# Optimization experiments

Measured on AMD Instinct MI355X. Metric: run time of the kernel, lower is better.

Reference implementation:

```python
import jax, jax.numpy as jnp
import numpy as np

TOP_K = 2
NUM_EXPERTS = 8
LB_COEFF = 0.01


def setup_inputs() -> dict:
    key = jax.random.key(0)
    ks = jax.random.split(key, 5)
    B, S, D, F, E = 4, 2048, 1024, 4096, NUM_EXPERTS
    s_in = 0.02
    return {
        "x": jax.random.normal(ks[0], (B, S, D), jnp.float32),
        "gate_w": jax.random.normal(ks[1], (D, E), jnp.float32) * s_in,
        "gate_b": jnp.zeros((E,), jnp.float32),
        "fc1_w": jax.random.normal(ks[2], (E, D, 2 * F), jnp.float32) * s_in,
        "fc1_b": jnp.zeros((E, 2 * F), jnp.float32),
        "fc2_w": jax.random.normal(ks[3], (E, F, D), jnp.float32) * s_in,
        "fc2_b": jnp.zeros((E, D), jnp.float32),
    }


def reference(x, gate_w, gate_b, fc1_w, fc1_b, fc2_w, fc2_b):
    B, S, D = x.shape
    E = gate_w.shape[1]
    xt = x.reshape(-1, D)                      # [T, D]
    T = xt.shape[0]

    gate_logits = xt @ gate_w + gate_b        # [T, E]
    gate_probs = jax.nn.softmax(gate_logits, axis=-1)
    top_w, top_i = jax.lax.top_k(gate_probs, TOP_K)      # [T, K]
    w_norm = top_w / (top_w.sum(-1, keepdims=True) + 1e-6)

    rows = jnp.arange(T)[:, None]
    # per-token per-expert combine weight (0 if expert not in top-k)
    combine = jnp.zeros((T, E), xt.dtype).at[rows, top_i].add(w_norm)  # [T, E]

    out = jnp.zeros_like(xt)
    for e in range(E):  # fixed small expert loop; each is a dense GEMM
        h = xt @ fc1_w[e] + fc1_b[e]                      # [T, 2F]
        a, g = jnp.split(h, 2, axis=-1)
        act = a * jax.nn.gelu(g, approximate=False)       # SwiGLU (exact gelu, torch default)
        y = act @ fc2_w[e] + fc2_b[e]                     # [T, D]
        out = out + combine[:, e:e + 1] * y

    chosen_mask = jnp.zeros((T, E), gate_probs.dtype).at[rows, top_i].set(1.0)
    frac = chosen_mask.mean(0)
    mean_probs = gate_probs.mean(0)
    lb_loss = LB_COEFF * E * jnp.sum(frac * mean_probs)

    return out.reshape(B, S, D), lb_loss
```

## Files before the change

### kernel.cpp

```cpp
#include <hip/hip_runtime.h>
#include <hip/hip_bf16.h>
#include <stdint.h>

typedef __attribute__((ext_vector_type(4))) float f32x4;
typedef __attribute__((ext_vector_type(8))) __bf16 bf16x8;
typedef __attribute__((ext_vector_type(4))) unsigned short u16x4;
typedef unsigned short u16;

#define NTOK 8192
#define DDIM 1024
#define FDIM 4096
#define NEXP 8

#define WS_XB    0ull
#define WS_W1T   (16777216ull)
#define WS_W2T   (WS_W1T + 134217728ull)
#define WS_ACT   (WS_W2T + 67108864ull)
#define WS_LIST  (WS_ACT + 142606336ull)
#define WS_PAIRW (WS_LIST + 262144ull)
#define WS_CNT   (WS_PAIRW + 262144ull)
#define WS_SUMP  (WS_CNT + 32ull)
#define WS_PAD   (WS_SUMP + 32ull)
#define WS_OFF   (WS_PAD + 32ull)
#define WS_T1E   (WS_OFF + 32ull)
#define WS_T1R   (WS_T1E + 512ull)
#define WS_T2E   (WS_T1R + 512ull)
#define WS_T2R   (WS_T2E + 1024ull)

static __device__ __forceinline__ u16 bf16rne(float f) {
  union { float f; uint32_t u; } c; c.f = f;
  return (u16)((c.u + 0x7FFFu + ((c.u >> 16) & 1u)) >> 16);
}

static __device__ __forceinline__ void load_lds16(const void* g, void* l) {
  __builtin_amdgcn_global_load_lds((const __attribute__((address_space(1))) void*)g,
                                   (__attribute__((address_space(3))) void*)l, 16, 0, 0);
}

__global__ __launch_bounds__(256) void gate_kernel(
    const float* __restrict__ x, const float* __restrict__ gw,
    const float* __restrict__ gb, u16* __restrict__ xb,
    int* __restrict__ cnt, float* __restrict__ sump,
    int* __restrict__ list, float* __restrict__ pairw) {
  const int tid = threadIdx.x;
  const int lane = tid & 63;
  const int wv = tid >> 6;
  const int t = blockIdx.x * 4 + wv;

  __shared__ float sp[8];
  if (tid < 8) sp[tid] = 0.f;
  __syncthreads();

  float acc[8] = {0.f,0.f,0.f,0.f,0.f,0.f,0.f,0.f};
  const float4* x4 = (const float4*)x + (size_t)t * 256;
  u16x4* xb4 = (u16x4*)xb + (size_t)t * 256;
  #pragma unroll
  for (int it = 0; it < 4; ++it) {
    const float4 xv = x4[it * 64 + lane];
    u16x4 bv;
    bv[0] = bf16rne(xv.x); bv[1] = bf16rne(xv.y);
    bv[2] = bf16rne(xv.z); bv[3] = bf16rne(xv.w);
    xb4[it * 64 + lane] = bv;
    const int d0 = (it * 64 + lane) * 4;
    #pragma unroll
    for (int j = 0; j < 4; ++j) {
      const float xs = (j == 0) ? xv.x : ((j == 1) ? xv.y : ((j == 2) ? xv.z : xv.w));
      const float* g = gw + (size_t)(d0 + j) * 8;
      #pragma unroll
      for (int e2 = 0; e2 < 8; ++e2) acc[e2] += xs * g[e2];
    }
  }
  #pragma unroll
  for (int e2 = 0; e2 < 8; ++e2) {
    float v = acc[e2];
    v += __shfl_xor(v, 1);  v += __shfl_xor(v, 2);  v += __shfl_xor(v, 4);
    v += __shfl_xor(v, 8);  v += __shfl_xor(v, 16); v += __shfl_xor(v, 32);
    acc[e2] = v;
  }
  float p[8]; float mx = -1e30f;
  #pragma unroll
  for (int e2 = 0; e2 < 8; ++e2) { p[e2] = acc[e2] + gb[e2]; mx = fmaxf(mx, p[e2]); }
  float s = 0.f;
  #pragma unroll
  for (int e2 = 0; e2 < 8; ++e2) { p[e2] = expf(p[e2] - mx); s += p[e2]; }
  const float inv = 1.f / s;
  #pragma unroll
  for (int e2 = 0; e2 < 8; ++e2) p[e2] *= inv;

  if (lane == 0) {
    int i1 = 0; float v1 = p[0];
    #pragma unroll
    for (int e2 = 1; e2 < 8; ++e2) if (p[e2] > v1) { v1 = p[e2]; i1 = e2; }
    int i2 = 0; float v2 = -1.f;
    #pragma unroll
    for (int e2 = 0; e2 < 8; ++e2) if (e2 != i1 && p[e2] > v2) { v2 = p[e2]; i2 = e2; }
    const float den = v1 + v2 + 1e-6f;
    const int p1 = atomicAdd(&cnt[i1], 1);
    list[i1 * NTOK + p1] = t; pairw[i1 * NTOK + p1] = v1 / den;
    const int p2 = atomicAdd(&cnt[i2], 1);
    list[i2 * NTOK + p2] = t; pairw[i2 * NTOK + p2] = v2 / den;
    #pragma unroll
    for (int e2 = 0; e2 < 8; ++e2) atomicAdd(&sp[e2], p[e2]);
  }
  __syncthreads();
  if (tid < 8) atomicAdd(&sump[tid], sp[tid]);
}

__global__ __launch_bounds__(256) void conv_transpose(
    const float* __restrict__ in, u16* __restrict__ out, int R, int C) {
  __shared__ float tile[64][65];
  const int e = blockIdx.z;
  const float* pin = in + (size_t)e * R * C;
  u16* pout = out + (size_t)e * R * C;
  const int tx = threadIdx.x & 15;
  const int ty = threadIdx.x >> 4;
  const int c0 = blockIdx.x * 64;
  const int r0 = blockIdx.y * 64;
  #pragma unroll
  for (int i = 0; i < 4; ++i) {
    const int r = ty + i * 16;
    const float4 v = *(const float4*)(pin + (size_t)(r0 + r) * C + c0 + tx * 4);
    tile[r][tx * 4 + 0] = v.x;
    tile[r][tx * 4 + 1] = v.y;
    tile[r][tx * 4 + 2] = v.z;
    tile[r][tx * 4 + 3] = v.w;
  }
  __syncthreads();
  #pragma unroll
  for (int i = 0; i < 4; ++i) {
    const int c = ty + i * 16;
    u16x4 o;
    o[0] = bf16rne(tile[tx * 4 + 0][c]);
    o[1] = bf16rne(tile[tx * 4 + 1][c]);
    o[2] = bf16rne(tile[tx * 4 + 2][c]);
    o[3] = bf16rne(tile[tx * 4 + 3][c]);
    *(u16x4*)(pout + (size_t)(c0 + c) * R + r0 + tx * 4) = o;
  }
}

__global__ void route_finalize(const int* __restrict__ cnt, const float* __restrict__ sump,
                               int* __restrict__ padc, int* __restrict__ offs,
                               int* __restrict__ list, float* __restrict__ pairw,
                               int* __restrict__ t1e, int* __restrict__ t1r,
                               int* __restrict__ t2e, int* __restrict__ t2r,
                               float* __restrict__ lb_out) {
  __shared__ int s_c[8], s_p[8];
  const int tid = threadIdx.x;
  if (tid == 0) {
    int o = 0; float lb = 0.f;
    for (int e = 0; e < 8; ++e) {
      const int c = cnt[e];
      const int pc = (c + 127) & ~127;
      s_c[e] = c; s_p[e] = pc;
      padc[e] = pc; offs[e] = o; o += pc;
      lb += ((float)c / 8192.f) * (sump[e] / 8192.f);
    }
    lb_out[0] = 0.01f * 8.f * lb;
    int n1 = 0;
    for (int e = 0; e < 8; ++e)
      for (int r = 0; r < s_p[e]; r += 256) { t1e[n1] = e; t1r[n1] = r; ++n1; }
    for (; n1 < 72; ++n1) { t1e[n1] = -1; t1r[n1] = 0; }
    int n2 = 0;
    for (int e = 0; e < 8; ++e)
      for (int r = 0; r < s_p[e]; r += 256) { t2e[n2] = e; t2r[n2] = r; ++n2; }
    for (; n2 < 72; ++n2) { t2e[n2] = -1; t2r[n2] = 0; }
  }
  __syncthreads();
  for (int e = 0; e < 8; ++e)
    for (int pq = s_c[e] + tid; pq < s_p[e]; pq += blockDim.x) {
      list[e * NTOK + pq] = 0; pairw[e * NTOK + pq] = 0.f;
    }
}

#define G1_NT 16
__global__ __launch_bounds__(512, 2) void gemm1_kernel(
    const u16* __restrict__ xb, const u16* __restrict__ w1t,
    const float* __restrict__ b1, const int* __restrict__ list,
    const int* __restrict__ padc, const int* __restrict__ offs,
    const int* __restrict__ t1e, const int* __restrict__ t1r,
    u16* __restrict__ act) {
  const int tt = blockIdx.y;
  const int e = t1e[tt];
  if (e < 0) return;
  const int row0 = t1r[tt];
  const int j = blockIdx.x;
  const int pc = padc[e];
  const int off_e = offs[e];

  __shared__ u16 lds[65536];

  const int tid = threadIdx.x;
  const int lane = tid & 63;
  const int wv = tid >> 6;
  const int wr = wv >> 2, wc = wv & 3;
  const int l15 = lane & 15, l4 = lane >> 4;

  const int rt0 = tid >> 2, rt1 = rt0 + 128;
  const int ce = ((tid & 3) ^ ((rt0 >> 1) & 3)) * 8;
  const int slot0 = row0 + rt0, slot1 = row0 + rt1;
  const int tok0 = (slot0 < pc) ? list[e * NTOK + slot0] : 0;
  const int tok1 = (slot1 < pc) ? list[e * NTOK + slot1] : 0;
  const u16* srcA0 = xb + (size_t)tok0 * DDIM + ce;
  const u16* srcA1 = xb + (size_t)tok1 * DDIM + ce;
  const int gn0 = j * 128 + (rt0 >> 5) * 16 + (rt0 & 15) + ((rt0 >> 4) & 1) * FDIM;
  const int gn1 = j * 128 + (rt1 >> 5) * 16 + (rt1 & 15) + ((rt1 >> 4) & 1) * FDIM;
  const u16* srcB0 = w1t + ((size_t)e * 2 * FDIM + gn0) * DDIM + ce;
  const u16* srcB1 = w1t + ((size_t)e * 2 * FDIM + gn1) * DDIM + ce;

  const int kel = (l4 ^ ((l15 >> 1) & 3)) * 8;
  const int aBase = (wr * 128 + l15) * 32 + kel;
  const int bBase = (wc * 64 + l15) * 32 + kel;

  f32x4 acc[8][4];
  #pragma unroll
  for (int m = 0; m < 8; ++m)
    #pragma unroll
    for (int n = 0; n < 4; ++n) { acc[m][n][0]=0.f; acc[m][n][1]=0.f; acc[m][n][2]=0.f; acc[m][n][3]=0.f; }

  #define STAGE_A(buf, kk, kt) do { \
    u16* _d = &lds[(buf) * 16384 + (kk) * 8192 + wv * 512]; \
    load_lds16(srcA0 + (kt) * 64 + (kk) * 32, _d); \
    load_lds16(srcA1 + (kt) * 64 + (kk) * 32, _d + 4096); \
  } while (0)
  #define STAGE_B(buf, kk, kt) do { \
    u16* _d = &lds[32768 + (buf) * 16384 + (kk) * 8192 + wv * 512]; \
    load_lds16(srcB0 + (kt) * 64 + (kk) * 32, _d); \
    load_lds16(srcB1 + (kt) * 64 + (kk) * 32, _d + 4096); \
  } while (0)

  STAGE_A(0, 0, 0); STAGE_B(0, 0, 0); STAGE_A(0, 1, 0); STAGE_B(0, 1, 0);
  STAGE_A(1, 0, 1); STAGE_B(1, 0, 1); STAGE_A(1, 1, 1);
  asm volatile("s_waitcnt vmcnt(6)" ::: "memory");
  __builtin_amdgcn_s_barrier();

  bf16x8 aF[8];
  for (int t = 0; t < G1_NT; ++t) {
    const int cur = t & 1;
    const int Ac0 = cur * 16384, Ac1 = Ac0 + 8192;
    const int Bc0 = 32768 + cur * 16384, Bc1 = Bc0 + 8192;
    {
      #pragma unroll
      for (int m = 0; m < 8; ++m) aF[m] = *(const bf16x8*)&lds[Ac0 + aBase + m * 512];
      bf16x8 b0 = *(const bf16x8*)&lds[Bc0 + bBase + 0 * 512];
      bf16x8 b1f = *(const bf16x8*)&lds[Bc0 + bBase + 1 * 512];
      __builtin_amdgcn_sched_barrier(0);
      if (t + 1 < G1_NT) STAGE_B(cur ^ 1, 1, t + 1);
      __builtin_amdgcn_s_barrier();
      __builtin_amdgcn_s_setprio(1);
      #pragma unroll
      for (int m = 0; m < 8; ++m) {
        acc[m][0] = __builtin_amdgcn_mfma_f32_16x16x32_bf16(aF[m], b0, acc[m][0], 0, 0, 0);
        acc[m][1] = __builtin_amdgcn_mfma_f32_16x16x32_bf16(aF[m], b1f, acc[m][1], 0, 0, 0);
      }
      __builtin_amdgcn_s_setprio(0);
      __builtin_amdgcn_s_barrier();
    }
    {
      bf16x8 b2 = *(const bf16x8*)&lds[Bc0 + bBase + 2 * 512];
      bf16x8 b3 = *(const bf16x8*)&lds[Bc0 + bBase + 3 * 512];
      __builtin_amdgcn_sched_barrier(0);
      if (t + 2 < G1_NT) STAGE_A(cur, 0, t + 2);
      __builtin_amdgcn_s_barrier();
      __builtin_amdgcn_s_setprio(1);
      #pragma unroll
      for (int m = 0; m < 8; ++m) {
        acc[m][2] = __builtin_amdgcn_mfma_f32_16x16x32_bf16(aF[m], b2, acc[m][2], 0, 0, 0);
        acc[m][3] = __builtin_amdgcn_mfma_f32_16x16x32_bf16(aF[m], b3, acc[m][3], 0, 0, 0);
      }
      __builtin_amdgcn_s_setprio(0);
      __builtin_amdgcn_s_barrier();
    }
    {
      #pragma unroll
      for (int m = 0; m < 8; ++m) aF[m] = *(const bf16x8*)&lds[Ac1 + aBase + m * 512];
      bf16x8 b0 = *(const bf16x8*)&lds[Bc1 + bBase + 0 * 512];
      bf16x8 b1f = *(const bf16x8*)&lds[Bc1 + bBase + 1 * 512];
      __builtin_amdgcn_sched_barrier(0);
      if (t + 2 < G1_NT) STAGE_B(cur, 0, t + 2);
      __builtin_amdgcn_s_barrier();
      __builtin_amdgcn_s_setprio(1);
      #pragma unroll
      for (int m = 0; m < 8; ++m) {
        acc[m][0] = __builtin_amdgcn_mfma_f32_16x16x32_bf16(aF[m], b0, acc[m][0], 0, 0, 0);
        acc[m][1] = __builtin_amdgcn_mfma_f32_16x16x32_bf16(aF[m], b1f, acc[m][1], 0, 0, 0);
      }
      __builtin_amdgcn_s_setprio(0);
      __builtin_amdgcn_s_barrier();
    }
    {
      bf16x8 b2 = *(const bf16x8*)&lds[Bc1 + bBase + 2 * 512];
      bf16x8 b3 = *(const bf16x8*)&lds[Bc1 + bBase + 3 * 512];
      __builtin_amdgcn_sched_barrier(0);
      if (t + 2 < G1_NT) STAGE_A(cur, 1, t + 2);
      __builtin_amdgcn_s_barrier();
      __builtin_amdgcn_s_setprio(1);
      #pragma unroll
      for (int m = 0; m < 8; ++m) {
        acc[m][2] = __builtin_amdgcn_mfma_f32_16x16x32_bf16(aF[m], b2, acc[m][2], 0, 0, 0);
        acc[m][3] = __builtin_amdgcn_mfma_f32_16x16x32_bf16(aF[m], b3, acc[m][3], 0, 0, 0);
      }
      __builtin_amdgcn_s_setprio(0);
      if (t < G1_NT - 1) {
        if (t == G1_NT - 2) asm volatile("s_waitcnt vmcnt(0)" ::: "memory");
        else                asm volatile("s_waitcnt vmcnt(6)" ::: "memory");
      }
      __builtin_amdgcn_s_barrier();
    }
  }
  #undef STAGE_A
  #undef STAGE_B

  const int rowlim = pc - row0;
  const size_t actrow0 = (size_t)(off_e + row0);
  #pragma unroll
  for (int p2 = 0; p2 < 2; ++p2) {
    const int col = j * 128 + (wc * 2 + p2) * 16 + l15;
    const float ba = b1[e * (2 * FDIM) + col];
    const float bg = b1[e * (2 * FDIM) + FDIM + col];
    #pragma unroll
    for (int m = 0; m < 8; ++m) {
      #pragma unroll
      for (int jr = 0; jr < 4; ++jr) {
        const int row = wr * 128 + m * 16 + l4 * 4 + jr;
        if (row < rowlim) {
          const float a = acc[m][2 * p2][jr] + ba;
          const float g = acc[m][2 * p2 + 1][jr] + bg;
          const float u = 0.7978845608028654f * (g + 0.044715f * g * g * g);
          const float ex = __expf(2.f * u);
          const float th = 1.f - 2.f / (ex + 1.f);
          const float gg = 0.5f * g * (1.f + th);
          act[(actrow0 + row) * FDIM + col] = bf16rne(a * gg);
        }
      }
    }
  }
}

#define G2_NT 64
__global__ __launch_bounds__(512, 2) void gemm2_kernel(
    const u16* __restrict__ act, const u16* __restrict__ w2t,
    const float* __restrict__ b2, const int* __restrict__ list,
    const float* __restrict__ pairw, const int* __restrict__ padc,
    const int* __restrict__ offs,
    const int* __restrict__ t2e, const int* __restrict__ t2r,
    float* __restrict__ out) {
  const int tt = blockIdx.x;
  const int e = t2e[tt];
  if (e < 0) return;
  const int row0 = t2r[tt];
  const int jt = blockIdx.y;
  const int pc = padc[e];
  const int off_e = offs[e];

  __shared__ u16 lds[49152];

  const int tid = threadIdx.x;
  const int lane = tid & 63;
  const int wv = tid >> 6;
  const int wr = wv >> 2, wc = wv & 3;
  const int l15 = lane & 15, l4 = lane >> 4;

  const int rt0 = tid >> 2, rt1 = rt0 + 128;
  const int ce = ((tid & 3) ^ ((rt0 >> 1) & 3)) * 8;
  const u16* srcA0 = act + (size_t)(off_e + row0 + rt0) * FDIM + ce;
  const u16* srcA1 = act + (size_t)(off_e + row0 + rt1) * FDIM + ce;
  const u16* srcB0 = w2t + ((size_t)e * DDIM + jt * 128 + rt0) * FDIM + ce;

  const int kel = (l4 ^ ((l15 >> 1) & 3)) * 8;
  const int aBase = (wr * 128 + l15) * 32 + kel;
  const int bBase = (wc * 32 + l15) * 32 + kel;

  f32x4 acc[8][2];
  #pragma unroll
  for (int m = 0; m < 8; ++m)
    #pragma unroll
    for (int n = 0; n < 2; ++n) { acc[m][n][0]=0.f; acc[m][n][1]=0.f; acc[m][n][2]=0.f; acc[m][n][3]=0.f; }

  #define STAGE2_A(buf, kk, kt) do { \
    u16* _d = &lds[(buf) * 16384 + (kk) * 8192 + wv * 512]; \
    load_lds16(srcA0 + (kt) * 64 + (kk) * 32, _d); \
    load_lds16(srcA1 + (kt) * 64 + (kk) * 32, _d + 4096); \
  } while (0)
  #define STAGE2_B(buf, kk, kt) do { \
    u16* _d = &lds[32768 + (buf) * 8192 + (kk) * 4096 + wv * 512]; \
    load_lds16(srcB0 + (kt) * 64 + (kk) * 32, _d); \
  } while (0)

  STAGE2_B(0, 0, 0); STAGE2_A(0, 0, 0); STAGE2_B(0, 1, 0); STAGE2_A(0, 1, 0);
  STAGE2_B(1, 0, 1); STAGE2_A(1, 0, 1); STAGE2_B(1, 1, 1);
  asm volatile("s_waitcnt vmcnt(4)" ::: "memory");
  __builtin_amdgcn_s_barrier();

  bf16x8 aF0[4], aF1[4];
  for (int t = 0; t < G2_NT; ++t) {
    const int cur = t & 1;
    const int Ac0 = cur * 16384, Ac1 = Ac0 + 8192;
    const int Bc0 = 32768 + cur * 8192, Bc1 = Bc0 + 4096;
    bf16x8 b0, b1f;
    {
      #pragma unroll
      for (int m = 0; m < 4; ++m) aF0[m] = *(const bf16x8*)&lds[Ac0 + aBase + m * 512];
      b0  = *(const bf16x8*)&lds[Bc0 + bBase + 0 * 512];
      b1f = *(const bf16x8*)&lds[Bc0 + bBase + 1 * 512];
      __builtin_amdgcn_sched_barrier(0);
      if (t + 1 < G2_NT) STAGE2_A(cur ^ 1, 1, t + 1);
      __builtin_amdgcn_s_barrier();
      __builtin_amdgcn_s_setprio(1);
      #pragma unroll
      for (int m = 0; m < 4; ++m) {
        acc[m][0] = __builtin_amdgcn_mfma_f32_16x16x32_bf16(aF0[m], b0, acc[m][0], 0, 0, 0);
        acc[m][1] = __builtin_amdgcn_mfma_f32_16x16x32_bf16(aF0[m], b1f, acc[m][1], 0, 0, 0);
      }
      __builtin_amdgcn_s_setprio(0);
      __builtin_amdgcn_s_barrier();
    }
    {
      #pragma unroll
      for (int m = 0; m < 4; ++m) aF1[m] = *(const bf16x8*)&lds[Ac0 + aBase + (m + 4) * 512];
      __builtin_amdgcn_sched_barrier(0);
      if (t + 2 < G2_NT) STAGE2_B(cur, 0, t + 2);
      __builtin_amdgcn_s_barrier();
      __builtin_amdgcn_s_setprio(1);
      #pragma unroll
      for (int m = 0; m < 4; ++m) {
        acc[m + 4][0] = __builtin_amdgcn_mfma_f32_16x16x32_bf16(aF1[m], b0, acc[m + 4][0], 0, 0, 0);
        acc[m + 4][1] = __builtin_amdgcn_mfma_f32_16x16x32_bf16(aF1[m], b1f, acc[m + 4][1], 0, 0, 0);
      }
      __builtin_amdgcn_s_setprio(0);
      __builtin_amdgcn_s_barrier();
    }
    {
      #pragma unroll
      for (int m = 0; m < 4; ++m) aF0[m] = *(const bf16x8*)&lds[Ac1 + aBase + m * 512];
      b0  = *(const bf16x8*)&lds[Bc1 + bBase + 0 * 512];
      b1f = *(const bf16x8*)&lds[Bc1 + bBase + 1 * 512];
      __builtin_amdgcn_sched_barrier(0);
      if (t + 2 < G2_NT) STAGE2_A(cur, 0, t + 2);
      __builtin_amdgcn_s_barrier();
      __builtin_amdgcn_s_setprio(1);
      #pragma unroll
      for (int m = 0; m < 4; ++m) {
        acc[m][0] = __builtin_amdgcn_mfma_f32_16x16x32_bf16(aF0[m], b0, acc[m][0], 0, 0, 0);
        acc[m][1] = __builtin_amdgcn_mfma_f32_16x16x32_bf16(aF0[m], b1f, acc[m][1], 0, 0, 0);
      }
      __builtin_amdgcn_s_setprio(0);
      __builtin_amdgcn_s_barrier();
    }
    {
      #pragma unroll
      for (int m = 0; m < 4; ++m) aF1[m] = *(const bf16x8*)&lds[Ac1 + aBase + (m + 4) * 512];
      __builtin_amdgcn_sched_barrier(0);
      if (t + 2 < G2_NT) STAGE2_B(cur, 1, t + 2);
      __builtin_amdgcn_s_barrier();
      __builtin_amdgcn_s_setprio(1);
      #pragma unroll
      for (int m = 0; m < 4; ++m) {
        acc[m + 4][0] = __builtin_amdgcn_mfma_f32_16x16x32_bf16(aF1[m], b0, acc[m + 4][0], 0, 0, 0);
        acc[m + 4][1] = __builtin_amdgcn_mfma_f32_16x16x32_bf16(aF1[m], b1f, acc[m + 4][1], 0, 0, 0);
      }
      __builtin_amdgcn_s_setprio(0);
      if (t < G2_NT - 1) {
        if (t == G2_NT - 2) asm volatile("s_waitcnt vmcnt(0)" ::: "memory");
        else                asm volatile("s_waitcnt vmcnt(4)" ::: "memory");
      }
      __builtin_amdgcn_s_barrier();
    }
  }
  #undef STAGE2_A
  #undef STAGE2_B

  const int rowlim = pc - row0;
  #pragma unroll
  for (int m = 0; m < 8; ++m) {
    #pragma unroll
    for (int jr = 0; jr < 4; ++jr) {
      const int row = wr * 128 + m * 16 + l4 * 4 + jr;
      if (row < rowlim) {
        const int pos = row0 + row;
        const int tok = list[e * NTOK + pos];
        const float pw = pairw[e * NTOK + pos];
        if (pw != 0.f) {
          #pragma unroll
          for (int n = 0; n < 2; ++n) {
            const int col = jt * 128 + wc * 32 + n * 16 + l15;
            const float v = (acc[m][n][jr] + b2[e * DDIM + col]) * pw;
            atomicAdd(&out[(size_t)tok * DDIM + col], v);
          }
        }
      }
    }
  }
}

extern "C" void kernel_launch(void* const* d_in, const int* in_sizes, int n_in,
                              void* d_out, int out_size, void* d_ws, size_t ws_size,
                              hipStream_t stream) {
  const float* x   = (const float*)d_in[0];
  const float* gw  = (const float*)d_in[1];
  const float* gb  = (const float*)d_in[2];
  const float* f1w = (const float*)d_in[3];
  const float* f1b = (const float*)d_in[4];
  const float* f2w = (const float*)d_in[5];
  const float* f2b = (const float*)d_in[6];
  float* out = (float*)d_out;
  char* ws = (char*)d_ws;

  u16*   xb    = (u16*)(ws + WS_XB);
  u16*   w1t   = (u16*)(ws + WS_W1T);
  u16*   w2t   = (u16*)(ws + WS_W2T);
  u16*   act   = (u16*)(ws + WS_ACT);
  int*   list  = (int*)(ws + WS_LIST);
  float* pairw = (float*)(ws + WS_PAIRW);
  int*   cnt   = (int*)(ws + WS_CNT);
  float* sump  = (float*)(ws + WS_SUMP);
  int*   padc  = (int*)(ws + WS_PAD);
  int*   offs  = (int*)(ws + WS_OFF);
  int*   t1e   = (int*)(ws + WS_T1E);
  int*   t1r   = (int*)(ws + WS_T1R);
  int*   t2e   = (int*)(ws + WS_T2E);
  int*   t2r   = (int*)(ws + WS_T2R);

  (void)hipMemsetAsync(d_out, 0, (size_t)out_size * sizeof(float), stream);
  (void)hipMemsetAsync(ws + WS_CNT, 0, 64, stream);

  gate_kernel<<<NTOK / 4, 256, 0, stream>>>(x, gw, gb, xb, cnt, sump, list, pairw);
  conv_transpose<<<dim3(8192 / 64, 1024 / 64, 8), 256, 0, stream>>>(f1w, w1t, 1024, 8192);
  conv_transpose<<<dim3(1024 / 64, 4096 / 64, 8), 256, 0, stream>>>(f2w, w2t, 4096, 1024);
  route_finalize<<<1, 256, 0, stream>>>(cnt, sump, padc, offs, list, pairw,
                                        t1e, t1r, t2e, t2r, out + 8388608);
  gemm1_kernel<<<dim3(32, 72), 512, 0, stream>>>(xb, w1t, f1b, list, padc, offs, t1e, t1r, act);
  gemm2_kernel<<<dim3(72, 8), 512, 0, stream>>>(act, w2t, f2b, list, pairw, padc, offs, t2e, t2r, out);
}
```

Baseline: 1.090 ms.

## Software-pipeline LDS fragment loads across phases in both GEMMs and swap gemm2 grid axes

Both GEMM main loops are restructured so each phase computes on fragments loaded in an earlier phase. The next tile's A (and, in gemm2, B) fragments are prefetched from LDS after the final barrier so their latency overlaps MFMA work. Gemm1 now uses a 4x4 register-blocked pattern over M halves instead of 8x2 over N halves. Gemm2's grid is transposed so blocks sharing an activation row tile launch adjacently, which should improve L2 reuse of the act rows. The prefetching raises register pressure and depends on the barrier ordering staying correct.

Result: no change. 1.092 ms (+0.2%).

```diff
diff --git a/kernel.cpp b/kernel.cpp
--- a/kernel.cpp
+++ b/kernel.cpp
@@ -233,77 +233,85 @@
   asm volatile("s_waitcnt vmcnt(6)" ::: "memory");
   __builtin_amdgcn_s_barrier();
 
-  bf16x8 aF[8];
+  bf16x8 aLo[4], aHi[4];
+  bf16x8 bk[4];
+  #pragma unroll
+  for (int m = 0; m < 4; ++m) aLo[m] = *(const bf16x8*)&lds[0 + aBase + m * 512];
+  __builtin_amdgcn_sched_barrier(0);
+
   for (int t = 0; t < G1_NT; ++t) {
     const int cur = t & 1;
     const int Ac0 = cur * 16384, Ac1 = Ac0 + 8192;
     const int Bc0 = 32768 + cur * 16384, Bc1 = Bc0 + 8192;
     {
       #pragma unroll
-      for (int m = 0; m < 8; ++m) aF[m] = *(const bf16x8*)&lds[Ac0 + aBase + m * 512];
-      bf16x8 b0 = *(const bf16x8*)&lds[Bc0 + bBase + 0 * 512];
-      bf16x8 b1f = *(const bf16x8*)&lds[Bc0 + bBase + 1 * 512];
+      for (int n = 0; n < 4; ++n) bk[n] = *(const bf16x8*)&lds[Bc0 + bBase + n * 512];
+      #pragma unroll
+      for (int m = 0; m < 4; ++m) aHi[m] = *(const bf16x8*)&lds[Ac0 + aBase + (m + 4) * 512];
       __builtin_amdgcn_sched_barrier(0);
       if (t + 1 < G1_NT) STAGE_B(cur ^ 1, 1, t + 1);
       __builtin_amdgcn_s_barrier();
       __builtin_amdgcn_s_setprio(1);
       #pragma unroll
-      for (int m = 0; m < 8; ++m) {
-        acc[m][0] = __builtin_amdgcn_mfma_f32_16x16x32_bf16(aF[m], b0, acc[m][0], 0, 0, 0);
-        acc[m][1] = __builtin_amdgcn_mfma_f32_16x16x32_bf16(aF[m], b1f, acc[m][1], 0, 0, 0);
-      }
-      __builtin_amdgcn_s_setprio(0);
-      __builtin_amdgcn_s_barrier();
-    }
-    {
-      bf16x8 b2 = *(const bf16x8*)&lds[Bc0 + bBase + 2 * 512];
-      bf16x8 b3 = *(const bf16x8*)&lds[Bc0 + bBase + 3 * 512];
+      for (int m = 0; m < 4; ++m)
+        #pragma unroll
+        for (int n = 0; n < 4; ++n)
+          acc[m][n] = __builtin_amdgcn_mfma_f32_16x16x32_bf16(aLo[m], bk[n], acc[m][n], 0, 0, 0);
+      __builtin_amdgcn_s_setprio(0);
+      __builtin_amdgcn_s_barrier();
+    }
+    {
+      #pragma unroll
+      for (int m = 0; m < 4; ++m) aLo[m] = *(const bf16x8*)&lds[Ac1 + aBase + m * 512];
       __builtin_amdgcn_sched_barrier(0);
       if (t + 2 < G1_NT) STAGE_A(cur, 0, t + 2);
       __builtin_amdgcn_s_barrier();
       __builtin_amdgcn_s_setprio(1);
       #pragma unroll
-      for (int m = 0; m < 8; ++m) {
-        acc[m][2] = __builtin_amdgcn_mfma_f32_16x16x32_bf16(aF[m], b2, acc[m][2], 0, 0, 0);
-        acc[m][3] = __builtin_amdgcn_mfma_f32_16x16x32_bf16(aF[m], b3, acc[m][3], 0, 0, 0);
-      }
-      __builtin_amdgcn_s_setprio(0);
-      __builtin_amdgcn_s_barrier();
-    }
-    {
-      #pragma unroll
-      for (int m = 0; m < 8; ++m) aF[m] = *(const bf16x8*)&lds[Ac1 + aBase + m * 512];
-      bf16x8 b0 = *(const bf16x8*)&lds[Bc1 + bBase + 0 * 512];
-      bf16x8 b1f = *(const bf16x8*)&lds[Bc1 + bBase + 1 * 512];
+      for (int m = 0; m < 4; ++m)
+        #pragma unroll
+        for (int n = 0; n < 4; ++n)
+          acc[m + 4][n] = __builtin_amdgcn_mfma_f32_16x16x32_bf16(aHi[m], bk[n], acc[m + 4][n], 0, 0, 0);
+      __builtin_amdgcn_s_setprio(0);
+      __builtin_amdgcn_s_barrier();
+    }
+    {
+      #pragma unroll
+      for (int n = 0; n < 4; ++n) bk[n] = *(const bf16x8*)&lds[Bc1 + bBase + n * 512];
+      #pragma unroll
+      for (int m = 0; m < 4; ++m) aHi[m] = *(const bf16x8*)&lds[Ac1 + aBase + (m + 4) * 512];
       __builtin_amdgcn_sched_barrier(0);
       if (t + 2 < G1_NT) STAGE_B(cur, 0, t + 2);
       __builtin_amdgcn_s_barrier();
       __builtin_amdgcn_s_setprio(1);
       #pragma unroll
-      for (int m = 0; m < 8; ++m) {
-        acc[m][0] = __builtin_amdgcn_mfma_f32_16x16x32_bf16(aF[m], b0, acc[m][0], 0, 0, 0);
-        acc[m][1] = __builtin_amdgcn_mfma_f32_16x16x32_bf16(aF[m], b1f, acc[m][1], 0, 0, 0);
-      }
-      __builtin_amdgcn_s_setprio(0);
-      __builtin_amdgcn_s_barrier();
-    }
-    {
-      bf16x8 b2 = *(const bf16x8*)&lds[Bc1 + bBase + 2 * 512];
-      bf16x8 b3 = *(const bf16x8*)&lds[Bc1 + bBase + 3 * 512];
-      __builtin_amdgcn_sched_barrier(0);
+      for (int m = 0; m < 4; ++m)
+        #pragma unroll
+        for (int n = 0; n < 4; ++n)
+          acc[m][n] = __builtin_amdgcn_mfma_f32_16x16x32_bf16(aLo[m], bk[n], acc[m][n], 0, 0, 0);
+      __builtin_amdgcn_s_setprio(0);
+      __builtin_amdgcn_s_barrier();
+    }
+    {
       if (t + 2 < G1_NT) STAGE_A(cur, 1, t + 2);
-      __builtin_amdgcn_s_barrier();
-      __builtin_amdgcn_s_setprio(1);
-      #pragma unroll
-      for (int m = 0; m < 8; ++m) {
-        acc[m][2] = __builtin_amdgcn_mfma_f32_16x16x32_bf16(aF[m], b2, acc[m][2], 0, 0, 0);
-        acc[m][3] = __builtin_amdgcn_mfma_f32_16x16x32_bf16(aF[m], b3, acc[m][3], 0, 0, 0);
-      }
-      __builtin_amdgcn_s_setprio(0);
       if (t < G1_NT - 1) {
         if (t == G1_NT - 2) asm volatile("s_waitcnt vmcnt(0)" ::: "memory");
         else                asm volatile("s_waitcnt vmcnt(6)" ::: "memory");
       }
+      __builtin_amdgcn_s_barrier();
+      if (t < G1_NT - 1) {
+        const int nAc0 = (cur ^ 1) * 16384;
+        #pragma unroll
+        for (int m = 0; m < 4; ++m) aLo[m] = *(const bf16x8*)&lds[nAc0 + aBase + m * 512];
+        __builtin_amdgcn_sched_barrier(0);
+      }
+      __builtin_amdgcn_s_setprio(1);
+      #pragma unroll
+      for (int m = 0; m < 4; ++m)
+        #pragma unroll
+        for (int n = 0; n < 4; ++n)
+          acc[m + 4][n] = __builtin_amdgcn_mfma_f32_16x16x32_bf16(aHi[m], bk[n], acc[m + 4][n], 0, 0, 0);
+      __builtin_amdgcn_s_setprio(0);
       __builtin_amdgcn_s_barrier();
     }
   }
@@ -344,11 +352,11 @@
     const int* __restrict__ offs,
     const int* __restrict__ t2e, const int* __restrict__ t2r,
     float* __restrict__ out) {
-  const int tt = blockIdx.x;
+  const int tt = blockIdx.y;
   const int e = t2e[tt];
   if (e < 0) return;
   const int row0 = t2r[tt];
-  const int jt = blockIdx.y;
+  const int jt = blockIdx.x;
   const int pc = padc[e];
   const int off_e = offs[e];
 
@@ -391,77 +399,95 @@
   asm volatile("s_waitcnt vmcnt(4)" ::: "memory");
   __builtin_amdgcn_s_barrier();
 
-  bf16x8 aF0[4], aF1[4];
+  bf16x8 aLo[4], aHi[4], bk0, bk1;
+  #pragma unroll
+  for (int m = 0; m < 4; ++m) aLo[m] = *(const bf16x8*)&lds[0 + aBase + m * 512];
+  bk0 = *(const bf16x8*)&lds[32768 + bBase + 0 * 512];
+  bk1 = *(const bf16x8*)&lds[32768 + bBase + 1 * 512];
+  __builtin_amdgcn_sched_barrier(0);
+
   for (int t = 0; t < G2_NT; ++t) {
     const int cur = t & 1;
     const int Ac0 = cur * 16384, Ac1 = Ac0 + 8192;
-    const int Bc0 = 32768 + cur * 8192, Bc1 = Bc0 + 4096;
-    bf16x8 b0, b1f;
-    {
-      #pragma unroll
-      for (int m = 0; m < 4; ++m) aF0[m] = *(const bf16x8*)&lds[Ac0 + aBase + m * 512];
-      b0  = *(const bf16x8*)&lds[Bc0 + bBase + 0 * 512];
-      b1f = *(const bf16x8*)&lds[Bc0 + bBase + 1 * 512];
+    const int Bc1 = 32768 + cur * 8192 + 4096;
+    {
+      #pragma unroll
+      for (int m = 0; m < 4; ++m) aHi[m] = *(const bf16x8*)&lds[Ac0 + aBase + (m + 4) * 512];
       __builtin_amdgcn_sched_barrier(0);
       if (t + 1 < G2_NT) STAGE2_A(cur ^ 1, 1, t + 1);
       __builtin_amdgcn_s_barrier();
       __builtin_amdgcn_s_setprio(1);
       #pragma unroll
       for (int m = 0; m < 4; ++m) {
-        acc[m][0] = __builtin_amdgcn_mfma_f32_16x16x32_bf16(aF0[m], b0, acc[m][0], 0, 0, 0);
-        acc[m][1] = __builtin_amdgcn_mfma_f32_16x16x32_bf16(aF0[m], b1f, acc[m][1], 0, 0, 0);
-      }
-      __builtin_amdgcn_s_setprio(0);
-      __builtin_amdgcn_s_barrier();
-    }
-    {
-      #pragma unroll
-      for (int m = 0; m < 4; ++m) aF1[m] = *(const bf16x8*)&lds[Ac0 + aBase + (m + 4) * 512];
+        acc[m][0] = __builtin_amdgcn_mfma_f32_16x16x32_bf16(aLo[m], bk0, acc[m][0], 0, 0, 0);
+        acc[m][1] = __builtin_amdgcn_mfma_f32_16x16x32_bf16(aLo[m], bk1, acc[m][1], 0, 0, 0);
+      }
+      __builtin_amdgcn_s_setprio(0);
+      __builtin_amdgcn_s_barrier();
+    }
+    {
+      #pragma unroll
+      for (int m = 0; m < 4; ++m) aLo[m] = *(const bf16x8*)&lds[Ac1 + aBase + m * 512];
       __builtin_amdgcn_sched_barrier(0);
       if (t + 2 < G2_NT) STAGE2_B(cur, 0, t + 2);
       __builtin_amdgcn_s_barrier();
       __builtin_amdgcn_s_setprio(1);
       #pragma unroll
       for (int m = 0; m < 4; ++m) {
-        acc[m + 4][0] = __builtin_amdgcn_mfma_f32_16x16x32_bf16(aF1[m], b0, acc[m + 4][0], 0, 0, 0);
-        acc[m + 4][1] = __builtin_amdgcn_mfma_f32_16x16x32_bf16(aF1[m], b1f, acc[m + 4][1], 0, 0, 0);
-      }
-      __builtin_amdgcn_s_setprio(0);
-      __builtin_amdgcn_s_barrier();
-    }
-    {
-      #pragma unroll
-      for (int m = 0; m < 4; ++m) aF0[m] = *(const bf16x8*)&lds[Ac1 + aBase + m * 512];
-      b0  = *(const bf16x8*)&lds[Bc1 + bBase + 0 * 512];
-      b1f = *(const bf16x8*)&lds[Bc1 + bBase + 1 * 512];
+        acc[m + 4][0] = __builtin_amdgcn_mfma_f32_16x16x32_bf16(aHi[m], bk0, acc[m + 4][0], 0, 0, 0);
+        acc[m + 4][1] = __builtin_amdgcn_mfma_f32_16x16x32_bf16(aHi[m], bk1, acc[m + 4][1], 0, 0, 0);
+      }
+      __builtin_amdgcn_s_setprio(0);
+      __builtin_amdgcn_s_barrier();
+    }
+    {
+      bk0 = *(const bf16x8*)&lds[Bc1 + bBase + 0 * 512];
+      bk1 = *(const bf16x8*)&lds[Bc1 + bBase + 1 * 512];
+      #pragma unroll
+      for (int m = 0; m < 4; ++m) aHi[m] = *(const bf16x8*)&lds[Ac1 + aBase + (m + 4) * 512];
       __builtin_amdgcn_sched_barrier(0);
       if (t + 2 < G2_NT) STAGE2_A(cur, 0, t + 2);
       __builtin_amdgcn_s_barrier();
       __builtin_amdgcn_s_setprio(1);
       #pragma unroll
       for (int m = 0; m < 4; ++m) {
-        acc[m][0] = __builtin_amdgcn_mfma_f32_16x16x32_bf16(aF0[m], b0, acc[m][0], 0, 0, 0);
-        acc[m][1] = __builtin_amdgcn_mfma_f32_16x16x32_bf16(aF0[m], b1f, acc[m][1], 0, 0, 0);
-      }
-      __builtin_amdgcn_s_setprio(0);
-      __builtin_amdgcn_s_barrier();
-    }
-    {
-      #pragma unroll
-      for (int m = 0; m < 4; ++m) aF1[m] = *(const bf16x8*)&lds[Ac1 + aBase + (m + 4) * 512];
-      __builtin_amdgcn_sched_barrier(0);
+        acc[m][0] = __builtin_amdgcn_mfma_f32_16x16x32_bf16(aLo[m], bk0, acc[m][0], 0, 0, 0);
+        acc[m][1] = __builtin_amdgcn_mfma_f32_16x16x32_bf16(aLo[m], bk1, acc[m][1], 0, 0, 0);
+      }
+      __builtin_amdgcn_s_setprio(0);
+      __builtin_amdgcn_s_barrier();
+    }
+    {
       if (t + 2 < G2_NT) STAGE2_B(cur, 1, t + 2);
-      __builtin_amdgcn_s_barrier();
-      __builtin_amdgcn_s_setprio(1);
-      #pragma unroll
-      for (int m = 0; m < 4; ++m) {
-        acc[m + 4][0] = __builtin_amdgcn_mfma_f32_16x16x32_bf16(aF1[m], b0, acc[m + 4][0], 0, 0, 0);
-        acc[m + 4][1] = __builtin_amdgcn_mfma_f32_16x16x32_bf16(aF1[m], b1f, acc[m + 4][1], 0, 0, 0);
-      }
-      __builtin_amdgcn_s_setprio(0);
       if (t < G2_NT - 1) {
         if (t == G2_NT - 2) asm volatile("s_waitcnt vmcnt(0)" ::: "memory");
         else                asm volatile("s_waitcnt vmcnt(4)" ::: "memory");
+      }
+      __builtin_amdgcn_s_barrier();
+      if (t < G2_NT - 1) {
+        const int nAc0 = (cur ^ 1) * 16384;
+        const int nBc0 = 32768 + (cur ^ 1) * 8192;
+        #pragma unroll
+        for (int m = 0; m < 4; ++m) aLo[m] = *(const bf16x8*)&lds[nAc0 + aBase + m * 512];
+        bf16x8 nb0 = *(const bf16x8*)&lds[nBc0 + bBase + 0 * 512];
+        bf16x8 nb1 = *(const bf16x8*)&lds[nBc0 + bBase + 1 * 512];
+        __builtin_amdgcn_sched_barrier(0);
+        __builtin_amdgcn_s_setprio(1);
+        #pragma unroll
+        for (int m = 0; m < 4; ++m) {
+          acc[m + 4][0] = __builtin_amdgcn_mfma_f32_16x16x32_bf16(aHi[m], bk0, acc[m + 4][0], 0, 0, 0);
+          acc[m + 4][1] = __builtin_amdgcn_mfma_f32_16x16x32_bf16(aHi[m], bk1, acc[m + 4][1], 0, 0, 0);
+        }
+        __builtin_amdgcn_s_setprio(0);
+        bk0 = nb0; bk1 = nb1;
+      } else {
+        __builtin_amdgcn_s_setprio(1);
+        #pragma unroll
+        for (int m = 0; m < 4; ++m) {
+          acc[m + 4][0] = __builtin_amdgcn_mfma_f32_16x16x32_bf16(aHi[m], bk0, acc[m + 4][0], 0, 0, 0);
+          acc[m + 4][1] = __builtin_amdgcn_mfma_f32_16x16x32_bf16(aHi[m], bk1, acc[m + 4][1], 0, 0, 0);
+        }
+        __builtin_amdgcn_s_setprio(0);
       }
       __builtin_amdgcn_s_barrier();
     }
@@ -529,5 +555,5 @@
   route_finalize<<<1, 256, 0, stream>>>(cnt, sump, padc, offs, list, pairw,
                                         t1e, t1r, t2e, t2r, out + 8388608);
   gemm1_kernel<<<dim3(32, 72), 512, 0, stream>>>(xb, w1t, f1b, list, padc, offs, t1e, t1r, act);
-  gemm2_kernel<<<dim3(72, 8), 512, 0, stream>>>(act, w2t, f2b, list, pairw, padc, offs, t2e, t2r, out);
-}
+  gemm2_kernel<<<dim3(8, 72), 512, 0, stream>>>(act, w2t, f2b, list, pairw, padc, offs, t2e, t2r, out);
+}
```

## Restructure GEMM main loops into two-phase register-prefetched pipeline and swap gemm2 grid order

Applied to the files above, without the earlier changes.

Both GEMM kernels move from four barrier-separated quarter-steps per K tile to two phases. Each phase holds a full K-half of A and B fragments in registers and prefetches the next half's fragments from LDS while the current MFMAs run, with global-to-LDS staging issued in larger batches. This halves the barrier count and overlaps LDS reads with MFMA work, at the cost of more VGPRs for the doubled fragment arrays, which may lower occupancy or cause spills under launch_bounds(512,2). The gemm2 grid is also transposed so the fast block index walks output columns, which changes the order in which blocks touch act and w2t and so their cache reuse.

After: 1.159 ms. 1.06x slower.

```diff
diff --git a/kernel.cpp b/kernel.cpp
--- a/kernel.cpp
+++ b/kernel.cpp
@@ -229,81 +229,62 @@
   } while (0)
 
   STAGE_A(0, 0, 0); STAGE_B(0, 0, 0); STAGE_A(0, 1, 0); STAGE_B(0, 1, 0);
-  STAGE_A(1, 0, 1); STAGE_B(1, 0, 1); STAGE_A(1, 1, 1);
-  asm volatile("s_waitcnt vmcnt(6)" ::: "memory");
+  STAGE_A(1, 0, 1); STAGE_B(1, 0, 1); STAGE_A(1, 1, 1); STAGE_B(1, 1, 1);
+  asm volatile("s_waitcnt vmcnt(8)" ::: "memory");
   __builtin_amdgcn_s_barrier();
 
-  bf16x8 aF[8];
+  bf16x8 aK0[8], aK1[8], bK0[4], bK1[4];
+  #pragma unroll
+  for (int m = 0; m < 8; ++m) aK0[m] = *(const bf16x8*)&lds[aBase + m * 512];
+  #pragma unroll
+  for (int n = 0; n < 4; ++n) bK0[n] = *(const bf16x8*)&lds[32768 + bBase + n * 512];
+  __builtin_amdgcn_sched_barrier(0);
+  __builtin_amdgcn_s_barrier();
+
   for (int t = 0; t < G1_NT; ++t) {
     const int cur = t & 1;
-    const int Ac0 = cur * 16384, Ac1 = Ac0 + 8192;
-    const int Bc0 = 32768 + cur * 16384, Bc1 = Bc0 + 8192;
+    const int Ac1 = cur * 16384 + 8192;
+    const int Bc1 = 32768 + cur * 16384 + 8192;
     {
       #pragma unroll
-      for (int m = 0; m < 8; ++m) aF[m] = *(const bf16x8*)&lds[Ac0 + aBase + m * 512];
-      bf16x8 b0 = *(const bf16x8*)&lds[Bc0 + bBase + 0 * 512];
-      bf16x8 b1f = *(const bf16x8*)&lds[Bc0 + bBase + 1 * 512];
+      for (int m = 0; m < 8; ++m) aK1[m] = *(const bf16x8*)&lds[Ac1 + aBase + m * 512];
+      #pragma unroll
+      for (int n = 0; n < 4; ++n) bK1[n] = *(const bf16x8*)&lds[Bc1 + bBase + n * 512];
       __builtin_amdgcn_sched_barrier(0);
-      if (t + 1 < G1_NT) STAGE_B(cur ^ 1, 1, t + 1);
+      if (t + 2 < G1_NT) { STAGE_A(cur, 0, t + 2); STAGE_B(cur, 0, t + 2); }
       __builtin_amdgcn_s_barrier();
       __builtin_amdgcn_s_setprio(1);
       #pragma unroll
-      for (int m = 0; m < 8; ++m) {
-        acc[m][0] = __builtin_amdgcn_mfma_f32_16x16x32_bf16(aF[m], b0, acc[m][0], 0, 0, 0);
-        acc[m][1] = __builtin_amdgcn_mfma_f32_16x16x32_bf16(aF[m], b1f, acc[m][1], 0, 0, 0);
-      }
+      for (int m = 0; m < 8; ++m)
+        #pragma unroll
+        for (int n = 0; n < 4; ++n)
+          acc[m][n] = __builtin_amdgcn_mfma_f32_16x16x32_bf16(aK0[m], bK0[n], acc[m][n], 0, 0, 0);
       __builtin_amdgcn_s_setprio(0);
       __builtin_amdgcn_s_barrier();
     }
     {
-      bf16x8 b2 = *(const bf16x8*)&lds[Bc0 + bBase + 2 * 512];
-      bf16x8 b3 = *(const bf16x8*)&lds[Bc0 + bBase + 3 * 512];
-      __builtin_amdgcn_sched_barrier(0);
-      if (t + 2 < G1_NT) STAGE_A(cur, 0, t + 2);
-      __builtin_amdgcn_s_barrier();
-      __builtin_amdgcn_s_setprio(1);
-      #pragma unroll
-      for (int m = 0; m < 8; ++m) {
-        acc[m][2] = __builtin_amdgcn_mfma_f32_16x16x32_bf16(aF[m], b2, acc[m][2], 0, 0, 0);
-        acc[m][3] = __builtin_amdgcn_mfma_f32_16x16x32_bf16(aF[m], b3, acc[m][3], 0, 0, 0);
-      }
-      __builtin_amdgcn_s_setprio(0);
-      __builtin_amdgcn_s_barrier();
-    }
-    {
-      #pragma unroll
-      for (int m = 0; m < 8; ++m) aF[m] = *(const bf16x8*)&lds[Ac1 + aBase + m * 512];
-      bf16x8 b0 = *(const bf16x8*)&lds[Bc1 + bBase + 0 * 512];
-      bf16x8 b1f = *(const bf16x8*)&lds[Bc1 + bBase + 1 * 512];
-      __builtin_amdgcn_sched_barrier(0);
-      if (t + 2 < G1_NT) STAGE_B(cur, 0, t + 2);
-      __builtin_amdgcn_s_barrier();
-      __builtin_amdgcn_s_setprio(1);
-      #pragma unroll
-      for (int m = 0; m < 8; ++m) {
-        acc[m][0] = __builtin_amdgcn_mfma_f32_16x16x32_bf16(aF[m], b0, acc[m][0], 0, 0, 0);
-        acc[m][1] = __builtin_amdgcn_mfma_f32_16x16x32_bf16(aF[m], b1f, acc[m][1], 0, 0, 0);
-      }
-      __builtin_amdgcn_s_setprio(0);
-      __builtin_amdgcn_s_barrier();
-    }
-    {
-      bf16x8 b2 = *(const bf16x8*)&lds[Bc1 + bBase + 2 * 512];
-      bf16x8 b3 = *(const bf16x8*)&lds[Bc1 + bBase + 3 * 512];
-      __builtin_amdgcn_sched_barrier(0);
-      if (t + 2 < G1_NT) STAGE_A(cur, 1, t + 2);
-      __builtin_amdgcn_s_barrier();
-      __builtin_amdgcn_s_setprio(1);
-      #pragma unroll
-      for (int m = 0; m < 8; ++m) {
-        acc[m][2] = __builtin_amdgcn_mfma_f32_16x16x32_bf16(aF[m], b2, acc[m][2], 0, 0, 0);
-        acc[m][3] = __builtin_amdgcn_mfma_f32_16x16x32_bf16(aF[m], b3, acc[m][3], 0, 0, 0);
-      }
-      __builtin_amdgcn_s_setprio(0);
+      if (t + 2 < G1_NT) { STAGE_A(cur, 1, t + 2); STAGE_B(cur, 1, t + 2); }
       if (t < G1_NT - 1) {
         if (t == G1_NT - 2) asm volatile("s_waitcnt vmcnt(0)" ::: "memory");
-        else                asm volatile("s_waitcnt vmcnt(6)" ::: "memory");
-      }
+        else                asm volatile("s_waitcnt vmcnt(8)" ::: "memory");
+      }
+      __builtin_amdgcn_s_barrier();
+      if (t + 1 < G1_NT) {
+        const int nA = (cur ^ 1) * 16384;
+        const int nB = 32768 + (cur ^ 1) * 16384;
+        #pragma unroll
+        for (int m = 0; m < 8; ++m) aK0[m] = *(const bf16x8*)&lds[nA + aBase + m * 512];
+        #pragma unroll
+        for (int n = 0; n < 4; ++n) bK0[n] = *(const bf16x8*)&lds[nB + bBase + n * 512];
+        __builtin_amdgcn_sched_barrier(0);
+      }
+      __builtin_amdgcn_s_setprio(1);
+      #pragma unroll
+      for (int m = 0; m < 8; ++m)
+        #pragma unroll
+        for (int n = 0; n < 4; ++n)
+          acc[m][n] = __builtin_amdgcn_mfma_f32_16x16x32_bf16(aK1[m], bK1[n], acc[m][n], 0, 0, 0);
+      __builtin_amdgcn_s_setprio(0);
       __builtin_amdgcn_s_barrier();
     }
   }
@@ -344,11 +325,11 @@
     const int* __restrict__ offs,
     const int* __restrict__ t2e, const int* __restrict__ t2r,
     float* __restrict__ out) {
-  const int tt = blockIdx.x;
+  const int tt = blockIdx.y;
   const int e = t2e[tt];
   if (e < 0) return;
   const int row0 = t2r[tt];
-  const int jt = blockIdx.y;
+  const int jt = blockIdx.x;
   const int pc = padc[e];
   const int off_e = offs[e];
 
@@ -386,83 +367,63 @@
     load_lds16(srcB0 + (kt) * 64 + (kk) * 32, _d); \
   } while (0)
 
-  STAGE2_B(0, 0, 0); STAGE2_A(0, 0, 0); STAGE2_B(0, 1, 0); STAGE2_A(0, 1, 0);
-  STAGE2_B(1, 0, 1); STAGE2_A(1, 0, 1); STAGE2_B(1, 1, 1);
-  asm volatile("s_waitcnt vmcnt(4)" ::: "memory");
+  STAGE2_A(0, 0, 0); STAGE2_B(0, 0, 0); STAGE2_A(0, 1, 0); STAGE2_B(0, 1, 0);
+  STAGE2_A(1, 0, 1); STAGE2_B(1, 0, 1); STAGE2_A(1, 1, 1); STAGE2_B(1, 1, 1);
+  asm volatile("s_waitcnt vmcnt(6)" ::: "memory");
   __builtin_amdgcn_s_barrier();
 
-  bf16x8 aF0[4], aF1[4];
+  bf16x8 aK0[8], aK1[8], bK0[2], bK1[2];
+  #pragma unroll
+  for (int m = 0; m < 8; ++m) aK0[m] = *(const bf16x8*)&lds[aBase + m * 512];
+  #pragma unroll
+  for (int n = 0; n < 2; ++n) bK0[n] = *(const bf16x8*)&lds[32768 + bBase + n * 512];
+  __builtin_amdgcn_sched_barrier(0);
+  __builtin_amdgcn_s_barrier();
+
   for (int t = 0; t < G2_NT; ++t) {
     const int cur = t & 1;
-    const int Ac0 = cur * 16384, Ac1 = Ac0 + 8192;
-    const int Bc0 = 32768 + cur * 8192, Bc1 = Bc0 + 4096;
-    bf16x8 b0, b1f;
+    const int Ac1 = cur * 16384 + 8192;
+    const int Bc1 = 32768 + cur * 8192 + 4096;
     {
       #pragma unroll
-      for (int m = 0; m < 4; ++m) aF0[m] = *(const bf16x8*)&lds[Ac0 + aBase + m * 512];
-      b0  = *(const bf16x8*)&lds[Bc0 + bBase + 0 * 512];
-      b1f = *(const bf16x8*)&lds[Bc0 + bBase + 1 * 512];
+      for (int m = 0; m < 8; ++m) aK1[m] = *(const bf16x8*)&lds[Ac1 + aBase + m * 512];
+      #pragma unroll
+      for (int n = 0; n < 2; ++n) bK1[n] = *(const bf16x8*)&lds[Bc1 + bBase + n * 512];
       __builtin_amdgcn_sched_barrier(0);
-      if (t + 1 < G2_NT) STAGE2_A(cur ^ 1, 1, t + 1);
+      if (t + 2 < G2_NT) { STAGE2_A(cur, 0, t + 2); STAGE2_B(cur, 0, t + 2); }
       __builtin_amdgcn_s_barrier();
       __builtin_amdgcn_s_setprio(1);
       #pragma unroll
-      for (int m = 0; m < 4; ++m) {
-        acc[m][0] = __builtin_amdgcn_mfma_f32_16x16x32_bf16(aF0[m], b0, acc[m][0], 0, 0, 0);
-        acc[m][1] = __builtin_amdgcn_mfma_f32_16x16x32_bf16(aF0[m], b1f, acc[m][1], 0, 0, 0);
+      for (int m = 0; m < 8; ++m) {
+        acc[m][0] = __builtin_amdgcn_mfma_f32_16x16x32_bf16(aK0[m], bK0[0], acc[m][0], 0, 0, 0);
+        acc[m][1] = __builtin_amdgcn_mfma_f32_16x16x32_bf16(aK0[m], bK0[1], acc[m][1], 0, 0, 0);
       }
       __builtin_amdgcn_s_setprio(0);
       __builtin_amdgcn_s_barrier();
     }
     {
-      #pragma unroll
-      for (int m = 0; m < 4; ++m) aF1[m] = *(const bf16x8*)&lds[Ac0 + aBase + (m + 4) * 512];
-      __builtin_amdgcn_sched_barrier(0);
-      if (t + 2 < G2_NT) STAGE2_B(cur, 0, t + 2);
-      __builtin_amdgcn_s_barrier();
-      __builtin_amdgcn_s_setprio(1);
-      #pragma unroll
-      for (int m = 0; m < 4; ++m) {
-        acc[m + 4][0] = __builtin_amdgcn_mfma_f32_16x16x32_bf16(aF1[m], b0, acc[m + 4][0], 0, 0, 0);
-        acc[m + 4][1] = __builtin_amdgcn_mfma_f32_16x16x32_bf16(aF1[m], b1f, acc[m + 4][1], 0, 0, 0);
-      }
-      __builtin_amdgcn_s_setprio(0);
-      __builtin_amdgcn_s_barrier();
-    }
-    {
-      #pragma unroll
-      for (int m = 0; m < 4; ++m) aF0[m] = *(const bf16x8*)&lds[Ac1 + aBase + m * 512];
-      b0  = *(const bf16x8*)&lds[Bc1 + bBase + 0 * 512];
-      b1f = *(const bf16x8*)&lds[Bc1 + bBase + 1 * 512];
-      __builtin_amdgcn_sched_barrier(0);
-      if (t + 2 < G2_NT) STAGE2_A(cur, 0, t + 2);
-      __builtin_amdgcn_s_barrier();
-      __builtin_amdgcn_s_setprio(1);
-      #pragma unroll
-      for (int m = 0; m < 4; ++m) {
-        acc[m][0] = __builtin_amdgcn_mfma_f32_16x16x32_bf16(aF0[m], b0, acc[m][0], 0, 0, 0);
-        acc[m][1] = __builtin_amdgcn_mfma_f32_16x16x32_bf16(aF0[m], b1f, acc[m][1], 0, 0, 0);
-      }
-      __builtin_amdgcn_s_setprio(0);
-      __builtin_amdgcn_s_barrier();
-    }
-    {
-      #pragma unroll
-      for (int m = 0; m < 4; ++m) aF1[m] = *(const bf16x8*)&lds[Ac1 + aBase + (m + 4) * 512];
-      __builtin_amdgcn_sched_barrier(0);
-      if (t + 2 < G2_NT) STAGE2_B(cur, 1, t + 2);
-      __builtin_amdgcn_s_barrier();
-      __builtin_amdgcn_s_setprio(1);
-      #pragma unroll
-      for (int m = 0; m < 4; ++m) {
-        acc[m + 4][0] = __builtin_amdgcn_mfma_f32_16x16x32_bf16(aF1[m], b0, acc[m + 4][0], 0, 0, 0);
-        acc[m + 4][1] = __builtin_amdgcn_mfma_f32_16x16x32_bf16(aF1[m], b1f, acc[m + 4][1], 0, 0, 0);
-      }
-      __builtin_amdgcn_s_setprio(0);
+      if (t + 2 < G2_NT) { STAGE2_A(cur, 1, t + 2); STAGE2_B(cur, 1, t + 2); }
       if (t < G2_NT - 1) {
         if (t == G2_NT - 2) asm volatile("s_waitcnt vmcnt(0)" ::: "memory");
-        else                asm volatile("s_waitcnt vmcnt(4)" ::: "memory");
-      }
+        else                asm volatile("s_waitcnt vmcnt(6)" ::: "memory");
+      }
+      __builtin_amdgcn_s_barrier();
+      if (t + 1 < G2_NT) {
+        const int nA = (cur ^ 1) * 16384;
+        const int nB = 32768 + (cur ^ 1) * 8192;
+        #pragma unroll
+        for (int m = 0; m < 8; ++m) aK0[m] = *(const bf16x8*)&lds[nA + aBase + m * 512];
+        #pragma unroll
+        for (int n = 0; n < 2; ++n) bK0[n] = *(const bf16x8*)&lds[nB + bBase + n * 512];
+        __builtin_amdgcn_sched_barrier(0);
+      }
+      __builtin_amdgcn_s_setprio(1);
+      #pragma unroll
+      for (int m = 0; m < 8; ++m) {
+        acc[m][0] = __builtin_amdgcn_mfma_f32_16x16x32_bf16(aK1[m], bK1[0], acc[m][0], 0, 0, 0);
+        acc[m][1] = __builtin_amdgcn_mfma_f32_16x16x32_bf16(aK1[m], bK1[1], acc[m][1], 0, 0, 0);
+      }
+      __builtin_amdgcn_s_setprio(0);
       __builtin_amdgcn_s_barrier();
     }
   }
@@ -529,5 +490,5 @@
   route_finalize<<<1, 256, 0, stream>>>(cnt, sump, padc, offs, list, pairw,
                                         t1e, t1r, t2e, t2r, out + 8388608);
   gemm1_kernel<<<dim3(32, 72), 512, 0, stream>>>(xb, w1t, f1b, list, padc, offs, t1e, t1r, act);
-  gemm2_kernel<<<dim3(72, 8), 512, 0, stream>>>(act, w2t, f2b, list, pairw, padc, offs, t2e, t2r, out);
-}
+  gemm2_kernel<<<dim3(8, 72), 512, 0, stream>>>(act, w2t, f2b, list, pairw, padc, offs, t2e, t2r, out);
+}
```
